# Performance work log

Hardware: AMD Instinct MI355X
Metric: run time of the kernel (lower is better)

Reference implementation:

```python
import jax, jax.numpy as jnp
import numpy as np
from jax.scipy.linalg import expm

B, D, K, H, DD, N_ITERS = 4096, 1024, 64, 64, 16, 2
LN_EPS = 1e-5


def _layernorm(x, g, b):
    m = jnp.mean(x, axis=-1, keepdims=True)
    v = jnp.mean((x - m) ** 2, axis=-1, keepdims=True)
    return (x - m) * jax.lax.rsqrt(v + LN_EPS) * g + b


def _rbf(x):
    # RBF kernel with median heuristic (lower median of positive upper-tri dist^2, torch-style)
    n = x.shape[0]
    xn = jnp.sum(x * x, axis=1, keepdims=True)
    d2 = jnp.clip(xn + xn.T - 2.0 * (x @ x.T), 0.0, None)  # [n,n]
    iu, ju = jnp.triu_indices(n, k=1)
    up = d2[iu, ju]
    mask = up > 0
    cnt = jnp.sum(mask)
    srt = jnp.sort(jnp.where(mask, up, jnp.inf))  # positives first, inf-padded
    med = srt[jnp.maximum((cnt - 1) // 2, 0)]
    sigma = jnp.maximum(jnp.where(cnt > 0, jnp.sqrt(med), 1.0), 1e-6)
    gamma = 1.0 / (2.0 * sigma * sigma)
    return jnp.exp(-gamma * d2)


def _center(k):
    # H K H with H = I - 1/n, expressed as double-centering (no extra [n,n] matmuls)
    return k - jnp.mean(k, axis=0, keepdims=True) - jnp.mean(k, axis=1, keepdims=True) + jnp.mean(k)


def _forward(features, ln_g, ln_b, W_u, b_u, W1, b1, W2, b2, adj_logits,
             dln_g, dln_b, W_db, b_db, W_mu, b_mu, W_lv, b_lv, eps):
    pooled = _layernorm(features, ln_g, ln_b)  # [B,D]
    A = jax.nn.sigmoid(adj_logits) * (1.0 - jnp.eye(K, dtype=adj_logits.dtype))  # [K,K]
    u = pooled @ W_u + b_u  # [B,K]

    # causal structural forward: K tiny 2->H->1 MLPs fused into batched einsums
    z = u
    for _ in range(N_ITERS):
        parents = z @ A  # [B,K]
        inp = jnp.stack([parents, u], axis=-1)  # [B,K,2]
        h = jax.nn.gelu(jnp.einsum('bkp,kph->bkh', inp, W1) + b1, approximate=False)  # [B,K,H]
        z = jnp.einsum('bkh,kh->bk', h, W2) + b2  # [B,K]
    z_c = z

    dh = jax.nn.gelu(_layernorm(features, dln_g, dln_b) @ W_db + b_db, approximate=False)  # [B,H]
    z_d_mu = dh @ W_mu + b_mu  # [B,DD]
    z_d_logvar = dh @ W_lv + b_lv  # [B,DD]
    z_d = z_d_mu + eps * jnp.exp(0.5 * z_d_logvar)

    domain_kl_loss = -0.5 * jnp.mean(jnp.sum(1.0 + z_d_logvar - z_d_mu ** 2 - jnp.exp(z_d_logvar), axis=-1))
    dag_loss = jnp.trace(expm(A * A)) - K

    kc = _rbf(z_c)
    kd = _rbf(z_d)
    n = z_c.shape[0]
    hsic_loss = jnp.sum(kc * _center(kd)) / (n - 1) ** 2  # tr(Kc H Kd H)/(n-1)^2

    return (z_c, z_d, z_d_mu, z_d_logvar, A, dag_loss, hsic_loss, domain_kl_loss)


def setup_inputs() -> dict:
    key = jax.random.key(0)
    ks = jax.random.split(key, 10)

    def rn(i, shape, scale):
        return jax.random.normal(ks[i], shape, jnp.float32) * scale

    return {
        'features': jax.random.normal(ks[0], (B, D), jnp.float32),
        'ln_g': jnp.ones((D,), jnp.float32),
        'ln_b': jnp.zeros((D,), jnp.float32),
        'W_u': rn(1, (D, K), 0.03),
        'b_u': jnp.zeros((K,), jnp.float32),
        'W1': rn(2, (K, 2, H), 0.5),
        'b1': jnp.zeros((K, H), jnp.float32),
        'W2': rn(3, (K, H), 0.12),
        'b2': jnp.zeros((K,), jnp.float32),
        'adj_logits': rn(4, (K, K), 1.0),
        'dln_g': jnp.ones((D,), jnp.float32),
        'dln_b': jnp.zeros((D,), jnp.float32),
        'W_db': rn(5, (D, H), 0.03),
        'b_db': jnp.zeros((H,), jnp.float32),
        'W_mu': rn(6, (H, DD), 0.12),
        'b_mu': jnp.zeros((DD,), jnp.float32),
        'W_lv': rn(7, (H, DD), 0.12),
        'b_lv': jnp.zeros((DD,), jnp.float32),
        'eps': jax.random.normal(ks[8], (B, DD), jnp.float32),
    }


def reference(features, ln_g, ln_b, W_u, b_u, W1, b1, W2, b2, adj_logits,
              dln_g, dln_b, W_db, b_db, W_mu, b_mu, W_lv, b_lv, eps):
    return _forward(features, ln_g, ln_b, W_u, b_u, W1, b1, W2, b2, adj_logits,
                    dln_g, dln_b, W_db, b_db, W_mu, b_mu, W_lv, b_lv, eps)
```

## Files before the change

kernel.cpp:

```cpp
#include <hip/hip_runtime.h>
#include <math.h>

#define NB 4096
#define ND 1024

#define O_ZC   0
#define O_ZD   262144
#define O_MU   327680
#define O_LV   393216
#define O_A    458752
#define O_DAG  462848
#define O_HSIC 462849
#define O_KL   462850

#define WS_H1C    256u
#define WS_H1D    1280u
#define WS_M2C    2304u
#define WS_M2D    35072u
#define WS_RSC    67840u
#define WS_RSD    84224u
#define WS_ZEND   100608u
#define WS_XNC    100608u
#define WS_XND    116992u
#define WS_WC     133376u
#define WS_CST    657664u
#define WS_W1T0   658176u
#define WS_W1T1   674560u
#define WS_B1T    690944u
#define WS_W2T    707328u
#define WS_U      723712u
#define WS_DH     1772288u

__device__ __forceinline__ float gelu_f(float x){
  float y = fabsf(x) * 0.70710678118654752440f;
  float t = 1.0f / (1.0f + 0.3275911f * y);
  float poly = t*(0.254829592f + t*(-0.284496736f + t*(1.421413741f + t*(-1.453152027f + t*1.061405429f))));
  float e = __expf(-y*y);
  float er = 1.0f - poly*e;
  float s = copysignf(er, x);
  return 0.5f * x * (1.0f + s);
}

__device__ __forceinline__ void tri_map(int b, int& bi, int& bj){
  int r = (int)((sqrtf(8.0f*(float)b + 1.0f) - 1.0f) * 0.5f);
  while ((r+1)*(r+2)/2 <= b) r++;
  while (r*(r+1)/2 > b) r--;
  bj = r; bi = b - r*(r+1)/2;
}

__device__ __forceinline__ void flush_hist(const unsigned* __restrict__ hist,
                                           unsigned long long* __restrict__ g,
                                           int n2, int t, int salt){
  for (int e = t; e < n2; e += 256){
    int idx = (e + salt) & (n2 - 1);
    unsigned lo = hist[2*idx], hi = hist[2*idx + 1];
    if (lo | hi)
      atomicAdd(&g[idx], (unsigned long long)lo | ((unsigned long long)hi << 32));
  }
}

__global__ __launch_bounds__(256) void k_zero(uint4* p, int n){
  uint4 z; z.x = 0; z.y = 0; z.z = 0; z.w = 0;
  for (int i = blockIdx.x*256 + threadIdx.x; i < n; i += gridDim.x*256) p[i] = z;
}

__global__ __launch_bounds__(256) void k_prep(
    const float* __restrict__ ln_g, const float* __restrict__ ln_b,
    const float* __restrict__ W_u,  const float* __restrict__ b_u,
    const float* __restrict__ dln_g,const float* __restrict__ dln_b,
    const float* __restrict__ W_db, const float* __restrict__ b_db,
    const float* __restrict__ adj,  const float* __restrict__ W1,
    const float* __restrict__ b1,   const float* __restrict__ W2,
    float* __restrict__ Wc, float* __restrict__ cst,
    float* __restrict__ w1t0, float* __restrict__ w1t1,
    float* __restrict__ b1t,  float* __restrict__ w2t,
    float* __restrict__ outA){
  __shared__ float red[256];
  int t = threadIdx.x, b = blockIdx.x;
  if (b < 512){
    int e = b*256 + t; int c = e & 127, d = e >> 7;
    Wc[e] = (c < 64) ? ln_g[d]*W_u[d*64 + c] : dln_g[d]*W_db[d*64 + (c-64)];
  } else if (b < 528){
    int e = (b-512)*256 + t; int i = e >> 6, j = e & 63;
    float a = 1.0f/(1.0f + __expf(-adj[e]));
    outA[e] = (i == j) ? 0.0f : a;
  } else if (b < 656){
    int col = b - 528;
    float p = 0.0f;
    for (int d = t; d < 1024; d += 256)
      p += (col < 64) ? ln_b[d]*W_u[d*64 + col] : dln_b[d]*W_db[d*64 + (col-64)];
    red[t] = p; __syncthreads();
    for (int off = 128; off > 0; off >>= 1){ if (t < off) red[t] += red[t+off]; __syncthreads(); }
    if (t == 0) cst[col] = red[0] + ((col < 64) ? b_u[col] : b_db[col-64]);
  } else {
    int e = (b-656)*256 + t; int which = e >> 12, r = e & 4095;
    int j = r >> 6, k = r & 63;
    if (which == 0)      w1t0[j*64+k] = W1[k*128 + j];
    else if (which == 1) w1t1[j*64+k] = W1[k*128 + 64 + j];
    else if (which == 2) b1t [j*64+k] = b1[k*64 + j];
    else                 w2t [j*64+k] = W2[k*64 + j];
  }
}

__global__ __launch_bounds__(512) void k_lngemm(const float* __restrict__ feat,
    const float* __restrict__ Wc, const float* __restrict__ cst,
    float* __restrict__ u_ws, float* __restrict__ dh_ws){
  __shared__ float xh[16][1024];
  int t = threadIdx.x, b = blockIdx.x;
  {
    int row = t >> 5, lane = t & 31;
    const float4* src = (const float4*)(feat + (b*16 + row)*1024);
    float4 v[8]; float s = 0.0f, s2 = 0.0f;
    #pragma unroll
    for (int q = 0; q < 8; q++){
      v[q] = src[lane + q*32];
      s += v[q].x + v[q].y + v[q].z + v[q].w;
      s2 = fmaf(v[q].x,v[q].x, fmaf(v[q].y,v[q].y, fmaf(v[q].z,v[q].z, fmaf(v[q].w,v[q].w, s2))));
    }
    #pragma unroll
    for (int off = 1; off < 32; off <<= 1){ s += __shfl_xor(s, off); s2 += __shfl_xor(s2, off); }
    float mean = s * (1.0f/1024.0f);
    float var  = s2 * (1.0f/1024.0f) - mean*mean;
    float rs = rsqrtf(var + 1e-5f);
    float4* dst = (float4*)&xh[row][0];
    #pragma unroll
    for (int q = 0; q < 8; q++){
      float4 w; w.x = (v[q].x-mean)*rs; w.y = (v[q].y-mean)*rs;
      w.z = (v[q].z-mean)*rs; w.w = (v[q].w-mean)*rs;
      dst[lane + q*32] = w;
    }
  }
  __syncthreads();
  int col = t & 127, rg = t >> 7;
  float acc[4] = {0,0,0,0};
  for (int d0 = 0; d0 < 1024; d0 += 4){
    float w0 = Wc[(d0  )*128 + col];
    float w1 = Wc[(d0+1)*128 + col];
    float w2 = Wc[(d0+2)*128 + col];
    float w3 = Wc[(d0+3)*128 + col];
    #pragma unroll
    for (int r = 0; r < 4; r++){
      float4 x = *(const float4*)&xh[rg*4 + r][d0];
      acc[r] = fmaf(x.x,w0, fmaf(x.y,w1, fmaf(x.z,w2, fmaf(x.w,w3, acc[r]))));
    }
  }
  float cc = cst[col];
  #pragma unroll
  for (int r = 0; r < 4; r++){
    int grow = b*16 + rg*4 + r;
    float o = acc[r] + cc;
    if (col < 64) u_ws[grow*64 + col] = o;
    else          dh_ws[grow*64 + (col-64)] = o;
  }
}

__global__ __launch_bounds__(256) void k_causal(const float* __restrict__ u_ws,
    const float* __restrict__ A_g, const float* __restrict__ w1t0g, const float* __restrict__ w1t1g,
    const float* __restrict__ b1tg, const float* __restrict__ w2tg, const float* __restrict__ b2_g,
    float* __restrict__ zc_out, float* __restrict__ xnc){
  __shared__ float w1t0[4096], w1t1[4096];
  __shared__ float zbuf[4][64];
  int t = threadIdx.x;
  for (int e = t; e < 4096; e += 256){ w1t0[e] = w1t0g[e]; w1t1[e] = w1t1g[e]; }
  int w = t >> 6, k = t & 63;
  int row = blockIdx.x*4 + w;
  float uu = u_ws[row*64 + k];
  float b2v = b2_g[k];
  float z = uu;
  __syncthreads();
  #pragma unroll
  for (int itr = 0; itr < 2; ++itr){
    zbuf[w][k] = z;
    float p0=0.f,p1=0.f,p2=0.f,p3=0.f;
    #pragma unroll
    for (int j0 = 0; j0 < 64; j0 += 4){
      float4 zz = *(const float4*)&zbuf[w][j0];
      p0 = fmaf(zz.x, A_g[(j0+0)*64 + k], p0);
      p1 = fmaf(zz.y, A_g[(j0+1)*64 + k], p1);
      p2 = fmaf(zz.z, A_g[(j0+2)*64 + k], p2);
      p3 = fmaf(zz.w, A_g[(j0+3)*64 + k], p3);
    }
    float p = (p0+p1)+(p2+p3);
    float a0=0.f, a1=0.f;
    #pragma unroll 8
    for (int j = 0; j < 64; j += 2){
      float pre0 = fmaf(p, w1t0[j*64+k],     fmaf(uu, w1t1[j*64+k],     b1tg[j*64+k]));
      float pre1 = fmaf(p, w1t0[(j+1)*64+k], fmaf(uu, w1t1[(j+1)*64+k], b1tg[(j+1)*64+k]));
      a0 = fmaf(gelu_f(pre0), w2tg[j*64+k],     a0);
      a1 = fmaf(gelu_f(pre1), w2tg[(j+1)*64+k], a1);
    }
    z = a0 + a1 + b2v;
  }
  zc_out[row*64 + k] = z;
  float sq = z*z;
  #pragma unroll
  for (int off = 1; off < 64; off <<= 1) sq += __shfl_xor(sq, off);
  if (k == 0) xnc[row] = sq;
}

__global__ __launch_bounds__(256) void k_domain(const float* __restrict__ dh_ws,
    const float* __restrict__ Wmu, const float* __restrict__ bmu,
    const float* __restrict__ Wlv, const float* __restrict__ blv,
    const float* __restrict__ eps, float* __restrict__ out, double* __restrict__ wsd,
    float* __restrict__ xnd){
  __shared__ float hb[4][64];
  int t = threadIdx.x, w = t >> 6, l = t & 63;
  int dd = l & 15;
  double klacc = 0.0;
  for (int it = 0; it < 4; ++it){
    int row = blockIdx.x*16 + it*4 + w;
    hb[w][l] = gelu_f(dh_ws[row*64 + l]);
    float val = 0.0f;
    if (l < 32){
      const float* W = (l < 16) ? Wmu : Wlv;
      float a = (l < 16) ? bmu[dd] : blv[dd];
      for (int j = 0; j < 64; j++) a = fmaf(hb[w][j], W[j*16 + dd], a);
      val = a;
    }
    float mu = __shfl(val, dd);
    float lv = __shfl(val, 16 + dd);
    float kle = 0.0f, zs = 0.0f;
    if (l < 16){
      out[O_MU + row*16 + dd] = mu;
      out[O_LV + row*16 + dd] = lv;
      float zdv = fmaf(eps[row*16 + dd], __expf(0.5f*lv), mu);
      out[O_ZD + row*16 + dd] = zdv;
      zs = zdv*zdv;
      kle = 1.0f + lv - mu*mu - __expf(lv);
    }
    #pragma unroll
    for (int off = 1; off < 16; off <<= 1){ kle += __shfl_xor(kle, off); zs += __shfl_xor(zs, off); }
    if (l == 0){ klacc += (double)kle; xnd[row] = zs; }
  }
  if (l == 0) atomicAdd(&wsd[1], klacc);
}

template<int DIM>
__device__ __forceinline__ void stageT(const float* __restrict__ src, float* __restrict__ dst,
                                       int i0, int t){
  for (int e = t; e < DIM*128; e += 256){
    int k = e & (DIM-1);
    int r = e >> (DIM == 64 ? 6 : 4);
    dst[k*128 + (r ^ ((k & 7) << 2))] = src[(i0 + r)*DIM + k];
  }
}

template<int KDIM>
__device__ __forceinline__ void dot8x8(const float* __restrict__ LA, const float* __restrict__ LB,
                                       int tx8, int ty8, float acc[8][8]){
  #pragma unroll 8
  for (int k = 0; k < KDIM; k++){
    int s = (k & 7) << 2;
    const float* pa = LA + k*128;
    const float* pb = LB + k*128;
    float4 a0 = *(const float4*)(pa + ((ty8    ) ^ s));
    float4 a1 = *(const float4*)(pa + ((ty8 + 4) ^ s));
    float4 b0 = *(const float4*)(pb + ((tx8    ) ^ s));
    float4 b1 = *(const float4*)(pb + ((tx8 + 4) ^ s));
    float av[8] = {a0.x,a0.y,a0.z,a0.w,a1.x,a1.y,a1.z,a1.w};
    float bv[8] = {b0.x,b0.y,b0.z,b0.w,b1.x,b1.y,b1.z,b1.w};
    #pragma unroll
    for (int ii = 0; ii < 8; ii++)
      #pragma unroll
      for (int jj = 0; jj < 8; jj++)
        acc[ii][jj] = fmaf(av[ii], bv[jj], acc[ii][jj]);
  }
}

__device__ void dag_mm(float* __restrict__ C, const float* __restrict__ Am, const float* __restrict__ Bm,
                       const float* __restrict__ Xm, float cI, float cX, int t, bool addG){
  int tx = t & 15, ty = t >> 4;
  float acc[4][4] = {};
  for (int k0 = 0; k0 < 64; k0 += 4){
    float4 a0 = *(const float4*)&Am[(ty*4+0)*64 + k0];
    float4 a1 = *(const float4*)&Am[(ty*4+1)*64 + k0];
    float4 a2 = *(const float4*)&Am[(ty*4+2)*64 + k0];
    float4 a3 = *(const float4*)&Am[(ty*4+3)*64 + k0];
    float4 b0 = *(const float4*)&Bm[(k0+0)*64 + tx*4];
    float4 b1 = *(const float4*)&Bm[(k0+1)*64 + tx*4];
    float4 b2 = *(const float4*)&Bm[(k0+2)*64 + tx*4];
    float4 b3 = *(const float4*)&Bm[(k0+3)*64 + tx*4];
#define MQ(ii, AV) \
    acc[ii][0] = fmaf(AV.x,b0.x, fmaf(AV.y,b1.x, fmaf(AV.z,b2.x, fmaf(AV.w,b3.x, acc[ii][0])))); \
    acc[ii][1] = fmaf(AV.x,b0.y, fmaf(AV.y,b1.y, fmaf(AV.z,b2.y, fmaf(AV.w,b3.y, acc[ii][1])))); \
    acc[ii][2] = fmaf(AV.x,b0.z, fmaf(AV.y,b1.z, fmaf(AV.z,b2.z, fmaf(AV.w,b3.z, acc[ii][2])))); \
    acc[ii][3] = fmaf(AV.x,b0.w, fmaf(AV.y,b1.w, fmaf(AV.z,b2.w, fmaf(AV.w,b3.w, acc[ii][3]))));
    MQ(0,a0) MQ(1,a1) MQ(2,a2) MQ(3,a3)
#undef MQ
  }
  #pragma unroll
  for (int ii = 0; ii < 4; ii++)
    #pragma unroll
    for (int jj = 0; jj < 4; jj++){
      int i = ty*4 + ii, j = tx*4 + jj;
      float v = acc[ii][jj];
      if (addG) v += ((i == j) ? cI : 0.0f) + cX * Xm[i*64 + j];
      C[i*64 + j] = v;
    }
  __syncthreads();
}

__device__ void dag_expm(float* ldsA, float* ldsB, const float* __restrict__ A_g,
                         float* __restrict__ dout){
  int t = threadIdx.x;
  float* X  = ldsA;
  float* X2 = ldsA + 4096;
  float* P  = ldsB;
  float* Pn = ldsB + 4096;
  for (int e = t; e < 4096; e += 256){ float a = A_g[e]; X[e] = a*a; }
  __syncthreads();
  int l = t & 63;
  float cs = 0.0f;
  for (int i = 0; i < 64; i++) cs += X[i*64 + l];
  #pragma unroll
  for (int off = 1; off < 64; off <<= 1) cs = fmaxf(cs, __shfl_xor(cs, off));
  int s_ = 0;
  if (cs > 2.0f) s_ = (int)ceilf(log2f(cs * 0.5f));
  if (s_ < 0) s_ = 0; if (s_ > 12) s_ = 12;
  float sc = exp2f((float)(-s_));
  __syncthreads();
  for (int e = t; e < 4096; e += 256) X[e] *= sc;
  __syncthreads();
  dag_mm(X2, X, X, X, 0.0f, 0.0f, t, false);
  const float C12 = 2.0876756987868099e-9f, C13 = 1.6059043836821613e-10f;
  for (int e = t; e < 4096; e += 256){
    int i = e >> 6, j = e & 63;
    P[e] = C13*X[e] + ((i == j) ? C12 : 0.0f);
  }
  __syncthreads();
  const float cf[12] = {1.0f, 1.0f, 0.5f, 1.0f/6.0f, 1.0f/24.0f, 1.0f/120.0f,
                        1.0f/720.0f, 1.0f/5040.0f, 1.0f/40320.0f, 1.0f/362880.0f,
                        1.0f/3628800.0f, 1.0f/39916800.0f};
  #pragma unroll
  for (int g = 5; g >= 0; --g){
    dag_mm(Pn, X2, P, X, cf[2*g], cf[2*g+1], t, true);
    float* tmp = P; P = Pn; Pn = tmp;
  }
  for (int q = 0; q < s_; ++q){
    dag_mm(Pn, P, P, X, 0.0f, 0.0f, t, false);
    float* tmp = P; P = Pn; Pn = tmp;
  }
  if (t < 64){
    float tr = P[t*65];
    #pragma unroll
    for (int off = 1; off < 64; off <<= 1) tr += __shfl_xor(tr, off);
    if (t == 0) dout[O_DAG] = tr - 64.0f;
  }
}

__global__ __launch_bounds__(256,1) void k_pass1(const float* __restrict__ out,
    const float* __restrict__ xnc, const float* __restrict__ xnd,
    unsigned* __restrict__ h1c, unsigned* __restrict__ h1d,
    float* __restrict__ dout){
  __shared__ __align__(16) float ldsA[8192];
  __shared__ __align__(16) float ldsB[8192];
  int t = threadIdx.x;
  if (blockIdx.x == 528){ dag_expm(ldsA, ldsB, out + O_A, dout); return; }
  int bi, bj; tri_map(blockIdx.x, bi, bj);
  bool diag = (bi == bj);
  int i0 = bi*128, j0 = bj*128;
  int tx = t & 15, ty = t >> 4, tx8 = tx*8, ty8 = ty*8;
  int rep = t & 31;
  unsigned* hist = (unsigned*)ldsA;
  stageT<64>(out + O_ZC, ldsA, i0, t);
  stageT<64>(out + O_ZC, ldsB, j0, t);
  float xi[8], xj[8];
  #pragma unroll
  for (int ii = 0; ii < 8; ii++){ xi[ii] = xnc[i0+ty8+ii]; xj[ii] = xnc[j0+tx8+ii]; }
  __syncthreads();
  float acc[8][8] = {};
  dot8x8<64>(ldsA, ldsB, tx8, ty8, acc);
  __syncthreads();
  for (int e = t; e < 8192; e += 256) hist[e] = 0u;
  __syncthreads();
  #pragma unroll
  for (int ii = 0; ii < 8; ii++)
    #pragma unroll
    for (int jj = 0; jj < 8; jj++){
      float d2 = xi[ii] + xj[jj] - 2.0f*acc[ii][jj];
      bool take = diag ? ((i0+ty8+ii) < (j0+tx8+jj)) : true;
      if (take && d2 > 0.0f)
        atomicAdd(&hist[((__float_as_uint(d2) >> 23) << 5) | rep], 1u);
    }
  __syncthreads();
  {
    int b = (t + blockIdx.x*37) & 255;
    unsigned s = 0;
    #pragma unroll
    for (int rr = 0; rr < 32; rr++) s += hist[(b << 5) | ((rr + t) & 31)];
    if (s) atomicAdd(&h1c[b], s);
  }
  __syncthreads();
  stageT<16>(out + O_ZD, ldsB, i0, t);
  stageT<16>(out + O_ZD, ldsB + 2048, j0, t);
  #pragma unroll
  for (int ii = 0; ii < 8; ii++){ xi[ii] = xnd[i0+ty8+ii]; xj[ii] = xnd[j0+tx8+ii]; }
  __syncthreads();
  float acd[8][8] = {};
  dot8x8<16>(ldsB, ldsB + 2048, tx8, ty8, acd);
  __syncthreads();
  for (int e = t; e < 8192; e += 256) hist[e] = 0u;
  __syncthreads();
  #pragma unroll
  for (int ii = 0; ii < 8; ii++)
    #pragma unroll
    for (int jj = 0; jj < 8; jj++){
      float d2 = xi[ii] + xj[jj] - 2.0f*acd[ii][jj];
      bool take = diag ? ((i0+ty8+ii) < (j0+tx8+jj)) : true;
      if (take && d2 > 0.0f)
        atomicAdd(&hist[((__float_as_uint(d2) >> 23) << 5) | rep], 1u);
    }
  __syncthreads();
  {
    int b = (t + blockIdx.x*53) & 255;
    unsigned s = 0;
    #pragma unroll
    for (int rr = 0; rr < 32; rr++) s += hist[(b << 5) | ((rr + t) & 31)];
    if (s) atomicAdd(&h1d[b], s);
  }
}

__device__ unsigned find_bin256(const unsigned* __restrict__ h1, unsigned* sbuf, int t,
                                unsigned* k2out){
  unsigned part = h1[t];
  sbuf[t] = part;
  __syncthreads();
  for (int off = 1; off < 256; off <<= 1){
    unsigned v = (t >= off) ? sbuf[t-off] : 0u;
    __syncthreads();
    sbuf[t] += v;
    __syncthreads();
  }
  unsigned total = sbuf[255];
  unsigned pre = sbuf[t] - part;
  __syncthreads();
  if (t == 0){ sbuf[0] = 0xFFFFFFFFu; sbuf[1] = 0u; }
  __syncthreads();
  if (total > 0){
    unsigned rt = (total - 1u) >> 1;
    if (rt >= pre && rt < pre + part){ sbuf[0] = (unsigned)t; sbuf[1] = rt - pre; }
  }
  __syncthreads();
  unsigned b1 = sbuf[0];
  unsigned k2 = sbuf[1];
  __syncthreads();
  if (k2out) *k2out = k2;
  return b1;
}

__global__ __launch_bounds__(256,1) void k_pass2(const float* __restrict__ out,
    const float* __restrict__ xnc, const float* __restrict__ xnd,
    const unsigned* __restrict__ h1c, const unsigned* __restrict__ h1d,
    unsigned long long* __restrict__ m2c, unsigned long long* __restrict__ m2d){
  __shared__ __align__(16) float ldsA[8192];
  __shared__ __align__(16) float ldsB[8192];
  unsigned* hist = (unsigned*)ldsA;
  int t = threadIdx.x;
  unsigned b1c = find_bin256(h1c, (unsigned*)ldsA, t, nullptr);
  unsigned b1d = find_bin256(h1d, (unsigned*)ldsA, t, nullptr);
  int bi, bj; tri_map(blockIdx.x, bi, bj);
  bool diag = (bi == bj);
  int i0 = bi*128, j0 = bj*128;
  int tx = t & 15, ty = t >> 4, tx8 = tx*8, ty8 = ty*8;
  stageT<64>(out + O_ZC, ldsA, i0, t);
  stageT<64>(out + O_ZC, ldsB, j0, t);
  float xi[8], xj[8];
  #pragma unroll
  for (int ii = 0; ii < 8; ii++){ xi[ii] = xnc[i0+ty8+ii]; xj[ii] = xnc[j0+tx8+ii]; }
  __syncthreads();
  float acc[8][8] = {};
  dot8x8<64>(ldsA, ldsB, tx8, ty8, acc);
  __syncthreads();
  for (int e = t; e < 8192; e += 256) hist[e] = 0u;
  __syncthreads();
  #pragma unroll
  for (int ii = 0; ii < 8; ii++)
    #pragma unroll
    for (int jj = 0; jj < 8; jj++){
      float d2 = xi[ii] + xj[jj] - 2.0f*acc[ii][jj];
      unsigned u = __float_as_uint(d2);
      bool take = (diag ? ((i0+ty8+ii) < (j0+tx8+jj)) : true) && d2 > 0.0f && (u >> 23) == b1c;
      if (take) atomicAdd(&hist[(u >> 10) & 0x1FFFu], 1u);
    }
  __syncthreads();
  flush_hist(hist, m2c, 4096, t, blockIdx.x * 37);
  __syncthreads();
  stageT<16>(out + O_ZD, ldsB, i0, t);
  stageT<16>(out + O_ZD, ldsB + 2048, j0, t);
  #pragma unroll
  for (int ii = 0; ii < 8; ii++){ xi[ii] = xnd[i0+ty8+ii]; xj[ii] = xnd[j0+tx8+ii]; }
  __syncthreads();
  float acd[8][8] = {};
  dot8x8<16>(ldsB, ldsB + 2048, tx8, ty8, acd);
  __syncthreads();
  for (int e = t; e < 8192; e += 256) hist[e] = 0u;
  __syncthreads();
  #pragma unroll
  for (int ii = 0; ii < 8; ii++)
    #pragma unroll
    for (int jj = 0; jj < 8; jj++){
      float d2 = xi[ii] + xj[jj] - 2.0f*acd[ii][jj];
      unsigned u = __float_as_uint(d2);
      bool take = (diag ? ((i0+ty8+ii) < (j0+tx8+jj)) : true) && d2 > 0.0f && (u >> 23) == b1d;
      if (take) atomicAdd(&hist[(u >> 10) & 0x1FFFu], 1u);
    }
  __syncthreads();
  flush_hist(hist, m2d, 4096, t, blockIdx.x * 53);
}

__global__ __launch_bounds__(256) void k_scan2(const unsigned* __restrict__ h1c,
    const unsigned* __restrict__ h1d, const unsigned* __restrict__ m2c,
    const unsigned* __restrict__ m2d, float* __restrict__ wsf){
  __shared__ unsigned sbuf[256];
  __shared__ unsigned res[2];
  int t = threadIdx.x;
  bool isd = blockIdx.x != 0;
  const unsigned* h1 = isd ? h1d : h1c;
  const unsigned* m2 = isd ? m2d : m2c;
  unsigned k2;
  unsigned b1 = find_bin256(h1, sbuf, t, &k2);
  if (b1 == 0xFFFFFFFFu){
    if (t == 0) wsf[8 + blockIdx.x] = 0.5f;
    return;
  }
  unsigned part = 0;
  #pragma unroll
  for (int i = 0; i < 32; i++) part += m2[t*32 + i];
  sbuf[t] = part; __syncthreads();
  for (int off = 1; off < 256; off <<= 1){
    unsigned v = (t >= off) ? sbuf[t-off] : 0u; __syncthreads(); sbuf[t] += v; __syncthreads();
  }
  unsigned pre = sbuf[t] - part;
  __syncthreads();
  if (t == 0) res[0] = 0u;
  __syncthreads();
  if (k2 >= pre && k2 < pre + part){
    unsigned run = pre;
    #pragma unroll
    for (int i = 0; i < 32; i++){
      unsigned c = m2[t*32 + i];
      if (k2 < run + c){ res[0] = (unsigned)(t*32 + i); break; }
      run += c;
    }
  }
  __syncthreads();
  if (t == 0){
    unsigned med_bits = (b1 << 23) | (res[0] << 10) | 512u;
    float med = __uint_as_float(med_bits);
    float sig = fmaxf(sqrtf(med), 1e-6f);
    wsf[8 + blockIdx.x] = 1.0f/(2.0f*sig*sig);
  }
}

__global__ __launch_bounds__(256,1) void k_hsic(const float* __restrict__ out,
    const float* __restrict__ xnc, const float* __restrict__ xnd,
    const float* __restrict__ wsf, double* __restrict__ wsd,
    float* __restrict__ rsc, float* __restrict__ rsd){
  __shared__ __align__(16) float ldsA[8192];
  __shared__ __align__(16) float ldsB[8192];
  int t = threadIdx.x;
  int bi, bj; tri_map(blockIdx.x, bi, bj);
  bool diag = (bi == bj);
  int i0 = bi*128, j0 = bj*128;
  int tx = t & 15, ty = t >> 4, tx8 = tx*8, ty8 = ty*8;
  float gc = wsf[8], gd = wsf[9];
  stageT<64>(out + O_ZC, ldsA, i0, t);
  stageT<64>(out + O_ZC, ldsB, j0, t);
  float xi[8], xj[8];
  #pragma unroll
  for (int ii = 0; ii < 8; ii++){ xi[ii] = xnc[i0+ty8+ii]; xj[ii] = xnc[j0+tx8+ii]; }
  __syncthreads();
  float kc[8][8] = {};
  dot8x8<64>(ldsA, ldsB, tx8, ty8, kc);
  #pragma unroll
  for (int ii = 0; ii < 8; ii++)
    #pragma unroll
    for (int jj = 0; jj < 8; jj++)
      kc[ii][jj] = __expf(-gc * fmaxf(xi[ii] + xj[jj] - 2.0f*kc[ii][jj], 0.0f));
  __syncthreads();
  stageT<16>(out + O_ZD, ldsA, i0, t);
  stageT<16>(out + O_ZD, ldsA + 2048, j0, t);
  #pragma unroll
  for (int ii = 0; ii < 8; ii++){ xi[ii] = xnd[i0+ty8+ii]; xj[ii] = xnd[j0+tx8+ii]; }
  __syncthreads();
  float ad[8][8] = {};
  dot8x8<16>(ldsA, ldsA + 2048, tx8, ty8, ad);
  float t1p = 0.0f;
  float rc[8] = {}, rd[8] = {}, cc[8] = {}, cd[8] = {};
  #pragma unroll
  for (int ii = 0; ii < 8; ii++)
    #pragma unroll
    for (int jj = 0; jj < 8; jj++){
      float kd = __expf(-gd * fmaxf(xi[ii] + xj[jj] - 2.0f*ad[ii][jj], 0.0f));
      float c = kc[ii][jj];
      t1p = fmaf(c, kd, t1p);
      rc[ii] += c; rd[ii] += kd;
      cc[jj] += c; cd[jj] += kd;
    }
  __syncthreads();
  float* red = ldsB;
  red[t] = 0.0f; red[t + 256] = 0.0f;
  __syncthreads();
  #pragma unroll
  for (int ii = 0; ii < 8; ii++){
    atomicAdd(&red[ty8 + ii], rc[ii]);
    atomicAdd(&red[128 + ty8 + ii], rd[ii]);
  }
  if (!diag){
    #pragma unroll
    for (int jj = 0; jj < 8; jj++){
      atomicAdd(&red[256 + tx8 + jj], cc[jj]);
      atomicAdd(&red[384 + tx8 + jj], cd[jj]);
    }
  }
  #pragma unroll
  for (int off = 1; off < 64; off <<= 1) t1p += __shfl_xor(t1p, off);
  if ((t & 63) == 0) red[512 + (t >> 6)] = t1p;
  __syncthreads();
  if (t < 128){ atomicAdd(&rsc[i0 + t], red[t]); atomicAdd(&rsd[i0 + t], red[128 + t]); }
  else if (!diag){ atomicAdd(&rsc[j0 + t - 128], red[256 + t - 128]); atomicAdd(&rsd[j0 + t - 128], red[384 + t - 128]); }
  if (t == 0){
    double s = (double)red[512] + (double)red[513] + (double)red[514] + (double)red[515];
    if (!diag) s *= 2.0;
    atomicAdd(&wsd[0], s);
  }
}

__global__ __launch_bounds__(256) void k_combine(const double* __restrict__ wsd,
    const float* __restrict__ rsc, const float* __restrict__ rsd, float* __restrict__ dout){
  __shared__ double r1[256], r2[256], r3[256];
  int t = threadIdx.x;
  double sc = 0.0, sd = 0.0, pp = 0.0;
  for (int i = t; i < 4096; i += 256){
    double a = rsc[i], b = rsd[i];
    sc += a; sd += b; pp += a*b;
  }
  r1[t] = sc; r2[t] = sd; r3[t] = pp; __syncthreads();
  for (int off = 128; off > 0; off >>= 1){
    if (t < off){ r1[t] += r1[t+off]; r2[t] += r2[t+off]; r3[t] += r3[t+off]; }
    __syncthreads();
  }
  if (t == 0){
    double n = 4096.0;
    double T1 = wsd[0];
    double hs = (T1 - 2.0*r3[0]/n + r1[0]*r2[0]/(n*n)) / ((n-1.0)*(n-1.0));
    dout[O_HSIC] = (float)hs;
    dout[O_KL]   = (float)(-0.5 * wsd[1] / n);
  }
}

extern "C" void kernel_launch(void* const* d_in, const int* in_sizes, int n_in,
                              void* d_out, int out_size, void* d_ws, size_t ws_size,
                              hipStream_t stream){
  (void)in_sizes; (void)n_in; (void)out_size; (void)ws_size;
  const float* feat  = (const float*)d_in[0];
  const float* ln_g  = (const float*)d_in[1];
  const float* ln_b  = (const float*)d_in[2];
  const float* W_u   = (const float*)d_in[3];
  const float* b_u   = (const float*)d_in[4];
  const float* W1    = (const float*)d_in[5];
  const float* b1    = (const float*)d_in[6];
  const float* W2    = (const float*)d_in[7];
  const float* b2    = (const float*)d_in[8];
  const float* adj   = (const float*)d_in[9];
  const float* dln_g = (const float*)d_in[10];
  const float* dln_b = (const float*)d_in[11];
  const float* W_db  = (const float*)d_in[12];
  const float* b_db  = (const float*)d_in[13];
  const float* W_mu  = (const float*)d_in[14];
  const float* b_mu  = (const float*)d_in[15];
  const float* W_lv  = (const float*)d_in[16];
  const float* b_lv  = (const float*)d_in[17];
  const float* eps   = (const float*)d_in[18];
  float* out = (float*)d_out;
  char* ws = (char*)d_ws;
  float*  wsf = (float*)ws;
  double* wsd = (double*)ws;
  unsigned* h1c  = (unsigned*)(ws + WS_H1C);
  unsigned* h1d  = (unsigned*)(ws + WS_H1D);
  unsigned* m2c  = (unsigned*)(ws + WS_M2C);
  unsigned* m2d  = (unsigned*)(ws + WS_M2D);
  float* rsc  = (float*)(ws + WS_RSC);
  float* rsd  = (float*)(ws + WS_RSD);
  float* xnc  = (float*)(ws + WS_XNC);
  float* xnd  = (float*)(ws + WS_XND);
  float* Wc   = (float*)(ws + WS_WC);
  float* cst  = (float*)(ws + WS_CST);
  float* w1t0 = (float*)(ws + WS_W1T0);
  float* w1t1 = (float*)(ws + WS_W1T1);
  float* b1t  = (float*)(ws + WS_B1T);
  float* w2t  = (float*)(ws + WS_W2T);
  float* u_ws = (float*)(ws + WS_U);
  float* dh_ws= (float*)(ws + WS_DH);

  k_zero<<<dim3(64), dim3(256), 0, stream>>>((uint4*)ws, (int)(WS_ZEND/16u));
  k_prep<<<dim3(720), dim3(256), 0, stream>>>(ln_g, ln_b, W_u, b_u, dln_g, dln_b, W_db, b_db,
                                              adj, W1, b1, W2, Wc, cst, w1t0, w1t1, b1t, w2t,
                                              out + O_A);
  k_lngemm<<<dim3(256), dim3(512), 0, stream>>>(feat, Wc, cst, u_ws, dh_ws);
  k_causal<<<dim3(1024), dim3(256), 0, stream>>>(u_ws, out + O_A, w1t0, w1t1, b1t, w2t, b2,
                                                 out + O_ZC, xnc);
  k_domain<<<dim3(256), dim3(256), 0, stream>>>(dh_ws, W_mu, b_mu, W_lv, b_lv, eps, out, wsd,
                                                xnd);
  k_pass1<<<dim3(529), dim3(256), 0, stream>>>(out, xnc, xnd, h1c, h1d, out);
  k_pass2<<<dim3(528), dim3(256), 0, stream>>>(out, xnc, xnd, h1c, h1d,
                                               (unsigned long long*)m2c,
                                               (unsigned long long*)m2d);
  k_scan2<<<dim3(2), dim3(256), 0, stream>>>(h1c, h1d, m2c, m2d, wsf);
  k_hsic<<<dim3(528), dim3(256), 0, stream>>>(out, xnc, xnd, wsf, wsd, rsc, rsd);
  k_combine<<<dim3(1), dim3(256), 0, stream>>>(wsd, rsc, rsd, out);
}
```

Baseline: 444.5 us.

## Replicate global median histograms and coarsen second-pass bins to cut atomic contention

Global histograms for the RBF median search are split into 8 replicas, chosen by block index, in both passes. Readers sum the replicas, which is meant to spread contention on global atomics. The second-pass fine histogram drops from 13 to 10 mantissa bits, with 8 per-lane LDS sub-copies to reduce LDS atomic conflicts and a much smaller flush. The trade-off is a coarser median estimate (bin midpoint at lower resolution) and extra reads of the replicas in the scan kernels.

```diff
diff --git a/kernel.cpp b/kernel.cpp
--- a/kernel.cpp
+++ b/kernel.cpp
@@ -14,22 +14,22 @@
 #define O_KL   462850
 
 #define WS_H1C    256u
-#define WS_H1D    1280u
-#define WS_M2C    2304u
-#define WS_M2D    35072u
-#define WS_RSC    67840u
-#define WS_RSD    84224u
-#define WS_ZEND   100608u
-#define WS_XNC    100608u
-#define WS_XND    116992u
-#define WS_WC     133376u
-#define WS_CST    657664u
-#define WS_W1T0   658176u
-#define WS_W1T1   674560u
-#define WS_B1T    690944u
-#define WS_W2T    707328u
-#define WS_U      723712u
-#define WS_DH     1772288u
+#define WS_H1D    8448u
+#define WS_M2C    16640u
+#define WS_M2D    49408u
+#define WS_RSC    82176u
+#define WS_RSD    98560u
+#define WS_ZEND   114944u
+#define WS_XNC    114944u
+#define WS_XND    131328u
+#define WS_WC     147712u
+#define WS_CST    672000u
+#define WS_W1T0   672512u
+#define WS_W1T1   688896u
+#define WS_B1T    705280u
+#define WS_W2T    721664u
+#define WS_U      738048u
+#define WS_DH     1786624u
 
 __device__ __forceinline__ float gelu_f(float x){
   float y = fabsf(x) * 0.70710678118654752440f;
@@ -46,17 +46,6 @@
   while ((r+1)*(r+2)/2 <= b) r++;
   while (r*(r+1)/2 > b) r--;
   bj = r; bi = b - r*(r+1)/2;
-}
-
-__device__ __forceinline__ void flush_hist(const unsigned* __restrict__ hist,
-                                           unsigned long long* __restrict__ g,
-                                           int n2, int t, int salt){
-  for (int e = t; e < n2; e += 256){
-    int idx = (e + salt) & (n2 - 1);
-    unsigned lo = hist[2*idx], hi = hist[2*idx + 1];
-    if (lo | hi)
-      atomicAdd(&g[idx], (unsigned long long)lo | ((unsigned long long)hi << 32));
-  }
 }
 
 __global__ __launch_bounds__(256) void k_zero(uint4* p, int n){
@@ -361,6 +350,7 @@
   int i0 = bi*128, j0 = bj*128;
   int tx = t & 15, ty = t >> 4, tx8 = tx*8, ty8 = ty*8;
   int rep = t & 31;
+  int xrep = (blockIdx.x & 7) * 256;
   unsigned* hist = (unsigned*)ldsA;
   stageT<64>(out + O_ZC, ldsA, i0, t);
   stageT<64>(out + O_ZC, ldsB, j0, t);
@@ -388,7 +378,7 @@
     unsigned s = 0;
     #pragma unroll
     for (int rr = 0; rr < 32; rr++) s += hist[(b << 5) | ((rr + t) & 31)];
-    if (s) atomicAdd(&h1c[b], s);
+    if (s) atomicAdd(&h1c[xrep + b], s);
   }
   __syncthreads();
   stageT<16>(out + O_ZD, ldsB, i0, t);
@@ -416,13 +406,15 @@
     unsigned s = 0;
     #pragma unroll
     for (int rr = 0; rr < 32; rr++) s += hist[(b << 5) | ((rr + t) & 31)];
-    if (s) atomicAdd(&h1d[b], s);
+    if (s) atomicAdd(&h1d[xrep + b], s);
   }
 }
 
 __device__ unsigned find_bin256(const unsigned* __restrict__ h1, unsigned* sbuf, int t,
                                 unsigned* k2out){
-  unsigned part = h1[t];
+  unsigned part = 0;
+  #pragma unroll
+  for (int r = 0; r < 8; r++) part += h1[r*256 + t];
   sbuf[t] = part;
   __syncthreads();
   for (int off = 1; off < 256; off <<= 1){
@@ -456,6 +448,8 @@
   __shared__ __align__(16) float ldsB[8192];
   unsigned* hist = (unsigned*)ldsA;
   int t = threadIdx.x;
+  int rep = t & 7;
+  int xrep = (blockIdx.x & 7) * 512;
   unsigned b1c = find_bin256(h1c, (unsigned*)ldsA, t, nullptr);
   unsigned b1d = find_bin256(h1d, (unsigned*)ldsA, t, nullptr);
   int bi, bj; tri_map(blockIdx.x, bi, bj);
@@ -480,10 +474,17 @@
       float d2 = xi[ii] + xj[jj] - 2.0f*acc[ii][jj];
       unsigned u = __float_as_uint(d2);
       bool take = (diag ? ((i0+ty8+ii) < (j0+tx8+jj)) : true) && d2 > 0.0f && (u >> 23) == b1c;
-      if (take) atomicAdd(&hist[(u >> 10) & 0x1FFFu], 1u);
-    }
-  __syncthreads();
-  flush_hist(hist, m2c, 4096, t, blockIdx.x * 37);
+      if (take) atomicAdd(&hist[(((u >> 13) & 0x3FFu) << 3) | rep], 1u);
+    }
+  __syncthreads();
+  for (int e = t; e < 512; e += 256){
+    int idx = (e + blockIdx.x*37) & 511;
+    unsigned lo = 0, hi = 0;
+    #pragma unroll
+    for (int rr = 0; rr < 8; rr++){ lo += hist[(2*idx)*8 + rr]; hi += hist[(2*idx+1)*8 + rr]; }
+    if (lo | hi)
+      atomicAdd(&m2c[xrep + idx], (unsigned long long)lo | ((unsigned long long)hi << 32));
+  }
   __syncthreads();
   stageT<16>(out + O_ZD, ldsB, i0, t);
   stageT<16>(out + O_ZD, ldsB + 2048, j0, t);
@@ -502,10 +503,17 @@
       float d2 = xi[ii] + xj[jj] - 2.0f*acd[ii][jj];
       unsigned u = __float_as_uint(d2);
       bool take = (diag ? ((i0+ty8+ii) < (j0+tx8+jj)) : true) && d2 > 0.0f && (u >> 23) == b1d;
-      if (take) atomicAdd(&hist[(u >> 10) & 0x1FFFu], 1u);
-    }
-  __syncthreads();
-  flush_hist(hist, m2d, 4096, t, blockIdx.x * 53);
+      if (take) atomicAdd(&hist[(((u >> 13) & 0x3FFu) << 3) | rep], 1u);
+    }
+  __syncthreads();
+  for (int e = t; e < 512; e += 256){
+    int idx = (e + blockIdx.x*53) & 511;
+    unsigned lo = 0, hi = 0;
+    #pragma unroll
+    for (int rr = 0; rr < 8; rr++){ lo += hist[(2*idx)*8 + rr]; hi += hist[(2*idx+1)*8 + rr]; }
+    if (lo | hi)
+      atomicAdd(&m2d[xrep + idx], (unsigned long long)lo | ((unsigned long long)hi << 32));
+  }
 }
 
 __global__ __launch_bounds__(256) void k_scan2(const unsigned* __restrict__ h1c,
@@ -523,9 +531,16 @@
     if (t == 0) wsf[8 + blockIdx.x] = 0.5f;
     return;
   }
+  unsigned bsum[4];
   unsigned part = 0;
   #pragma unroll
-  for (int i = 0; i < 32; i++) part += m2[t*32 + i];
+  for (int i = 0; i < 4; i++){
+    unsigned b = t*4 + i;
+    unsigned s = 0;
+    #pragma unroll
+    for (int r = 0; r < 8; r++) s += m2[r*1024 + b];
+    bsum[i] = s; part += s;
+  }
   sbuf[t] = part; __syncthreads();
   for (int off = 1; off < 256; off <<= 1){
     unsigned v = (t >= off) ? sbuf[t-off] : 0u; __syncthreads(); sbuf[t] += v; __syncthreads();
@@ -537,15 +552,14 @@
   if (k2 >= pre && k2 < pre + part){
     unsigned run = pre;
     #pragma unroll
-    for (int i = 0; i < 32; i++){
-      unsigned c = m2[t*32 + i];
-      if (k2 < run + c){ res[0] = (unsigned)(t*32 + i); break; }
-      run += c;
+    for (int i = 0; i < 4; i++){
+      if (k2 < run + bsum[i]){ res[0] = (unsigned)(t*4 + i); break; }
+      run += bsum[i];
     }
   }
   __syncthreads();
   if (t == 0){
-    unsigned med_bits = (b1 << 23) | (res[0] << 10) | 512u;
+    unsigned med_bits = (b1 << 23) | (res[0] << 13) | 4096u;
     float med = __uint_as_float(med_bits);
     float sig = fmaxf(sqrtf(med), 1e-6f);
     wsf[8 + blockIdx.x] = 1.0f/(2.0f*sig*sig);
```

Measured after the change: 412.9 us. 1.08x faster.
